# Performance work log

Measured on AMD Instinct MI355X. Metric: run time of the kernel, lower is better.

## Reference

```python
import jax, jax.numpy as jnp
import numpy as np

N = 100000
E = 1000000
P = 1000000
HID = 128
ROLE_VOCAB = 8
ROLE_DIM = 16
IDX_VOCAB = 1024
IDX_DIM = 8
FEAT = 14
IN_DIM = FEAT + IDX_DIM + ROLE_DIM  # 38


def setup_inputs() -> dict:
    key = jax.random.key(0)
    ks = jax.random.split(key, 20)
    s = 0.02
    return {
        "block_features": jax.random.normal(ks[0], (N, FEAT), jnp.float32),
        "role_ids": jax.random.randint(ks[1], (N,), 0, ROLE_VOCAB),
        "b2b_src": jax.random.randint(ks[2], (E,), 0, N),
        "b2b_dst": jax.random.randint(ks[3], (E,), 0, N),
        "b2b_w": jax.random.uniform(ks[4], (E,), jnp.float32),
        "p2b_block": jax.random.randint(ks[5], (P,), 0, N),
        "p2b_w": jax.random.uniform(ks[6], (P,), jnp.float32),
        "role_emb": jax.random.normal(ks[7], (ROLE_VOCAB, ROLE_DIM), jnp.float32),
        "idx_emb": jax.random.normal(ks[8], (IDX_VOCAB, IDX_DIM), jnp.float32),
        "W1": jax.random.normal(ks[9], (IN_DIM, HID), jnp.float32) * s,
        "b1": jnp.zeros((HID,), jnp.float32),
        "W2": jax.random.normal(ks[10], (HID, HID), jnp.float32) * s,
        "b2": jnp.zeros((HID,), jnp.float32),
        "M1": jax.random.normal(ks[11], (HID, HID), jnp.float32) * s,
        "mb1": jnp.zeros((HID,), jnp.float32),
        "M2": jax.random.normal(ks[12], (HID, HID), jnp.float32) * s,
        "mb2": jnp.zeros((HID,), jnp.float32),
        "ln_g": jnp.ones((HID,), jnp.float32),
        "ln_b": jnp.zeros((HID,), jnp.float32),
    }


def _layernorm(x, g, b, eps=1e-5):
    mu = jnp.mean(x, axis=-1, keepdims=True)
    var = jnp.mean(jnp.square(x - mu), axis=-1, keepdims=True)
    return (x - mu) * jax.lax.rsqrt(var + eps) * g + b


def reference(block_features, role_ids, b2b_src, b2b_dst, b2b_w, p2b_block, p2b_w,
              role_emb, idx_emb, W1, b1, W2, b2, M1, mb1, M2, mb2, ln_g, ln_b):
    n = block_features.shape[0]
    # embeddings + input MLP
    re = role_emb[role_ids]                                  # [N, 16]
    ie = idx_emb[jnp.arange(n) % IDX_VOCAB]                  # [N, 8]
    x = jnp.concatenate([block_features, re, ie], axis=-1)   # [N, 38]
    h = jax.nn.relu(x @ W1 + b1)
    emb = jax.nn.relu(h @ W2 + b2)                           # [N, HID]
    # b2b: symmetric weighted scatter-add of neighbor embeddings
    agg = jnp.zeros_like(emb)
    agg = agg.at[b2b_src].add(emb[b2b_dst] * b2b_w[:, None])
    agg = agg.at[b2b_dst].add(emb[b2b_src] * b2b_w[:, None])
    # p2b: agg[j] += emb[j] * w  ==  emb * (sum of pin weights per block)
    pw = jnp.zeros((n,), emb.dtype).at[p2b_block].add(p2b_w)
    agg = agg + emb * pw[:, None]
    # message MLP + residual + LayerNorm
    m = jax.nn.relu(agg @ M1 + mb1) @ M2 + mb2
    block_embeddings = _layernorm(emb + m, ln_g, ln_b)
    graph_embedding = jnp.mean(block_embeddings, axis=0)
    return block_embeddings, graph_embedding
```

## Files before the change

### kernel.cpp

```cpp
#include <hip/hip_runtime.h>

#define FEAT 14
#define ROLE_DIM 16
#define IDX_DIM 8
#define IN_DIM 38
#define HID 128
#define IDX_VOCAB 1024
#define BINN 128
#define NBINS_MAX 800
#define NSEG 1024
#define BINP_CAPT 8
#define BINP_SCAP 16
#define SORT_CAP 4096

typedef __attribute__((ext_vector_type(8))) short short8;
typedef __attribute__((ext_vector_type(4))) float f32x4;
typedef __attribute__((ext_vector_type(2))) float f32x2;

__device__ __forceinline__ ushort f2bf(float f) {
    uint u = __float_as_uint(f);
    return (ushort)((u + 0x7FFFu + ((u >> 16) & 1u)) >> 16);
}
__device__ __forceinline__ float bf2f(ushort h) {
    return __uint_as_float((uint)h << 16);
}
__device__ __forceinline__ uchar f2fp8(float f) {
    return (uchar)(__builtin_amdgcn_cvt_pk_fp8_f32(f, f, 0, false) & 0xff);
}

__global__ void k_prep(const float* __restrict__ W1, const float* __restrict__ W2,
                       const float* __restrict__ M1, const float* __restrict__ M2,
                       ushort* __restrict__ W1t, ushort* __restrict__ W2t,
                       ushort* __restrict__ M1t, ushort* __restrict__ M2t)
{
    int t = blockIdx.x * 256 + threadIdx.x;
    if (t < 8192) {
        int c = t >> 6, k = t & 63;
        W1t[t] = (k < IN_DIM) ? f2bf(W1[k * HID + c]) : (ushort)0;
    } else if (t < 24576) {
        int u = t - 8192; int c = u >> 7, k = u & 127;
        W2t[u] = f2bf(W2[k * HID + c]);
    } else if (t < 40960) {
        int u = t - 24576; int c = u >> 7, k = u & 127;
        M1t[u] = f2bf(M1[k * HID + c]);
    } else if (t < 57344) {
        int u = t - 40960; int c = u >> 7, k = u & 127;
        M2t[u] = f2bf(M2[k * HID + c]);
    }
}

#define LDSA 32768

__device__ __forceinline__ void embed_body(
    char* lds, int id,
    const float* __restrict__ feat, const int* __restrict__ role_ids,
    const float* __restrict__ role_emb, const float* __restrict__ idx_emb,
    const ushort* __restrict__ W1t, const float* __restrict__ b1,
    const ushort* __restrict__ W2t, const float* __restrict__ b2,
    ushort* __restrict__ embh, uchar* __restrict__ embf8, int N)
{
    const int tid = threadIdx.x;
    const int w = tid >> 6, l = tid & 63;
    const int li = l & 15, hi = l >> 4;
    const int base = id * 64;

    for (int c = 0; c < 4; ++c) {
        int idx = c * 256 + tid;
        int col = idx >> 3, ch = idx & 7;
        uint4 v = *(const uint4*)(W1t + col * 64 + ch * 8);
        *(uint4*)(lds + col * 256 + ((ch * 16) ^ ((col & 7) << 4))) = v;
    }
    {
        int row = tid >> 2, kq = (tid & 3) * 16;
        int gr = base + row; if (gr >= N) gr = N - 1;
        int rid = role_ids[gr];
        float xv[16];
        #pragma unroll
        for (int j = 0; j < 16; ++j) {
            int k = kq + j;
            float v = 0.0f;
            if (k < FEAT)                 v = feat[gr * FEAT + k];
            else if (k < FEAT + ROLE_DIM) v = role_emb[rid * ROLE_DIM + (k - FEAT)];
            else if (k < IN_DIM)          v = idx_emb[(gr & (IDX_VOCAB - 1)) * IDX_DIM + (k - FEAT - ROLE_DIM)];
            xv[j] = v;
        }
        uint p[8];
        #pragma unroll
        for (int j = 0; j < 8; ++j)
            p[j] = (uint)f2bf(xv[2 * j]) | ((uint)f2bf(xv[2 * j + 1]) << 16);
        char* db = lds + LDSA + row * 256;
        int sw = (row & 7) << 4;
        *(uint4*)(db + ((kq * 2) ^ sw))      = make_uint4(p[0], p[1], p[2], p[3]);
        *(uint4*)(db + ((kq * 2 + 16) ^ sw)) = make_uint4(p[4], p[5], p[6], p[7]);
    }
    __syncthreads();

    f32x4 C[8];
    #pragma unroll
    for (int ct = 0; ct < 8; ++ct) C[ct] = (f32x4){0.f, 0.f, 0.f, 0.f};
    {
        const int arow = w * 16 + li;
        const int asw = (arow & 7) << 4;
        #pragma unroll
        for (int ks = 0; ks < 2; ++ks) {
            short8 a = *(short8*)(lds + LDSA + arow * 256 + ((ks * 64 + hi * 16) ^ asw));
            #pragma unroll
            for (int ct = 0; ct < 8; ++ct) {
                int bcol = ct * 16 + li;
                short8 b = *(short8*)(lds + bcol * 256 + ((ks * 64 + hi * 16) ^ ((bcol & 7) << 4)));
                C[ct] = __builtin_amdgcn_mfma_f32_16x16x32_bf16(a, b, C[ct], 0, 0, 0);
            }
        }
    }
    __syncthreads();

    #pragma unroll
    for (int ct = 0; ct < 8; ++ct) {
        int col = ct * 16 + li;
        float bv = b1[col];
        #pragma unroll
        for (int r = 0; r < 4; ++r) {
            int hrow = w * 16 + hi * 4 + r;
            float h = fmaxf(C[ct][r] + bv, 0.0f);
            *(ushort*)(lds + LDSA + hrow * 256 + ((col * 2) ^ ((hrow & 7) << 4))) = f2bf(h);
        }
    }
    for (int c = 0; c < 8; ++c) {
        int idx = c * 256 + tid;
        int col = idx >> 4, ch = idx & 15;
        uint4 v = *(const uint4*)(W2t + col * 128 + ch * 8);
        *(uint4*)(lds + col * 256 + ((ch * 16) ^ ((col & 7) << 4))) = v;
    }
    __syncthreads();

    f32x4 C2[8];
    #pragma unroll
    for (int ct = 0; ct < 8; ++ct) C2[ct] = (f32x4){0.f, 0.f, 0.f, 0.f};
    {
        const int arow = w * 16 + li;
        const int asw = (arow & 7) << 4;
        #pragma unroll
        for (int ks = 0; ks < 4; ++ks) {
            short8 a = *(short8*)(lds + LDSA + arow * 256 + ((ks * 64 + hi * 16) ^ asw));
            #pragma unroll
            for (int ct = 0; ct < 8; ++ct) {
                int bcol = ct * 16 + li;
                short8 b = *(short8*)(lds + bcol * 256 + ((ks * 64 + hi * 16) ^ ((bcol & 7) << 4)));
                C2[ct] = __builtin_amdgcn_mfma_f32_16x16x32_bf16(a, b, C2[ct], 0, 0, 0);
            }
        }
    }

    #pragma unroll
    for (int ct = 0; ct < 8; ++ct) {
        int col = ct * 16 + li;
        float bv = b2[col];
        #pragma unroll
        for (int r = 0; r < 4; ++r) {
            int gr = base + w * 16 + hi * 4 + r;
            if (gr < N) {
                float o = fmaxf(C2[ct][r] + bv, 0.0f);
                embh[(size_t)gr * 128 + col] = f2bf(o);
                embf8[(size_t)gr * 128 + col] = f2fp8(o);
            }
        }
    }
}

__device__ __forceinline__ void binp_body(
    char* lds, int id,
    const int* __restrict__ src, const int* __restrict__ dst,
    const float* __restrict__ wgt, uint* __restrict__ staged,
    int* __restrict__ cnt,
    const int* __restrict__ pb, const float* __restrict__ pv,
    float* __restrict__ pw,
    int E, int P, int nbins, int chunkE, int chunkP)
{
    uint* buf   = (uint*)lds;
    int* curT   = (int*)(lds + 25600);
    const int tid = threadIdx.x;
    for (int i = tid; i < nbins; i += 256) curT[i] = 0;
    __syncthreads();

    const int lo = id * chunkE;
    const int hiE = (lo + chunkE) < E ? (lo + chunkE) : E;
    for (int i = lo + tid; i < hiE; i += 256) {
        int s = src[i], d = dst[i];
        uint q = (uint)(wgt[i] * 255.0f + 0.5f);
        int bs = s >> 7;
        uint es = ((uint)(s & 127) << 25) | ((uint)d << 8) | q;
        int ps = atomicAdd(&curT[bs], 1);
        if (ps < BINP_CAPT) buf[bs * BINP_CAPT + ps] = es;
        else if (ps < BINP_SCAP)
            staged[((size_t)bs * NSEG + id) * BINP_SCAP + ps] = es;
        int bd = d >> 7;
        uint ed = ((uint)(d & 127) << 25) | ((uint)s << 8) | q;
        int pd = atomicAdd(&curT[bd], 1);
        if (pd < BINP_CAPT) buf[bd * BINP_CAPT + pd] = ed;
        else if (pd < BINP_SCAP)
            staged[((size_t)bd * NSEG + id) * BINP_SCAP + pd] = ed;
    }
    __syncthreads();
    for (int b = tid; b < nbins; b += 256) {
        int tot = curT[b];
        int k = tot < BINP_CAPT ? tot : BINP_CAPT;
        uint* dp = staged + ((size_t)b * NSEG + id) * BINP_SCAP;
        for (int i = 0; i < k; ++i) dp[i] = buf[b * BINP_CAPT + i];
        cnt[id * nbins + b] = tot < BINP_SCAP ? tot : BINP_SCAP;
    }

    int loP = id * chunkP;
    int hiP = loP + chunkP; if (hiP > P) hiP = P;
    for (int i = loP + tid; i < hiP; i += 256)
        atomicAdd(&pw[pb[i]], pv[i]);
}

__global__ __launch_bounds__(256) void k_embed_binp(
    const float* __restrict__ feat, const int* __restrict__ role_ids,
    const float* __restrict__ role_emb, const float* __restrict__ idx_emb,
    const ushort* __restrict__ W1t, const float* __restrict__ b1,
    const ushort* __restrict__ W2t, const float* __restrict__ b2,
    ushort* __restrict__ embh, uchar* __restrict__ embf8,
    const int* __restrict__ src, const int* __restrict__ dst,
    const float* __restrict__ wgt, uint* __restrict__ staged,
    int* __restrict__ cnt,
    const int* __restrict__ pb, const float* __restrict__ pv,
    float* __restrict__ pw,
    int N, int E, int P, int nbins, int chunkE, int chunkP)
{
    __shared__ char lds[49152];
    const int bid = blockIdx.x;
    int role, id;
    if (bid < 2 * NSEG) { role = bid & 1; id = bid >> 1; }
    else                { role = 0; id = NSEG + (bid - 2 * NSEG); }

    if (role == 0)
        embed_body(lds, id, feat, role_ids, role_emb, idx_emb,
                   W1t, b1, W2t, b2, embh, embf8, N);
    else
        binp_body(lds, id, src, dst, wgt, staged, cnt, pb, pv, pw,
                  E, P, nbins, chunkE, chunkP);
}

__global__ __launch_bounds__(256) void k_agg(
    const uint* __restrict__ staged, const int* __restrict__ cnt,
    const ushort* __restrict__ embh, const uchar* __restrict__ embf8,
    const float* __restrict__ pw,
    ushort* __restrict__ aggh, int N, int nbins)
{
    __shared__ int hist[BINN];
    __shared__ int startL[BINN];
    __shared__ int curL[BINN];
    __shared__ int sc[BINN];
    __shared__ uint sorted[SORT_CAP];

    const int tid = threadIdx.x;
    const int b = blockIdx.x;
    const int baseNode = b << 7;

    if (tid < BINN) hist[tid] = 0;
    __syncthreads();

    int cSeg[4];
    #pragma unroll
    for (int ss = 0; ss < 4; ++ss) {
        int seg = ss * 256 + tid;
        cSeg[ss] = cnt[seg * nbins + b];
        const uint* sp = staged + ((size_t)b * NSEG + seg) * BINP_SCAP;
        for (int k = 0; k < cSeg[ss]; ++k)
            atomicAdd(&hist[sp[k] >> 25], 1);
    }
    __syncthreads();

    int v = (tid < BINN) ? hist[tid] : 0;
    if (tid < BINN) sc[tid] = v;
    __syncthreads();
    for (int off = 1; off < BINN; off <<= 1) {
        int u = (tid < BINN && tid >= off) ? sc[tid - off] : 0;
        __syncthreads();
        if (tid < BINN) sc[tid] += u;
        __syncthreads();
    }
    if (tid < BINN) {
        startL[tid] = sc[tid] - v;
        curL[tid]   = sc[tid] - v;
    }
    __syncthreads();

    #pragma unroll
    for (int ss = 0; ss < 4; ++ss) {
        int seg = ss * 256 + tid;
        const uint* sp = staged + ((size_t)b * NSEG + seg) * BINP_SCAP;
        for (int k = 0; k < cSeg[ss]; ++k) {
            uint e = sp[k];
            int pos = atomicAdd(&curL[e >> 25], 1);
            if (pos < SORT_CAP) sorted[pos] = e;
        }
    }
    __syncthreads();

    const int g  = tid >> 3;
    const int cg = tid & 7;
    const int c0 = cg * 16;
    for (int h = 0; h < 4; ++h) {
        int nl = h * 32 + g;
        int node = baseNode + nl;
        if (node < N) {
            float acc[16];
            float pwn = pw[node];
            const uint4* r = (const uint4*)(embh + ((size_t)node << 7) + c0);
            uint4 u0 = r[0], u1 = r[1];
            uint uu[8] = {u0.x, u0.y, u0.z, u0.w, u1.x, u1.y, u1.z, u1.w};
            #pragma unroll
            for (int j = 0; j < 8; ++j) {
                acc[2*j]   = __uint_as_float(uu[j] << 16) * pwn;
                acc[2*j+1] = __uint_as_float(uu[j] & 0xffff0000u) * pwn;
            }
            const int st = startL[nl], deg = hist[nl];
            #pragma unroll 4
            for (int i = 0; i < deg; ++i) {
                uint en = sorted[st + i];
                int nb   = (int)((en >> 8) & 0x1FFFFu);
                float wt = (float)(en & 255u) * (1.0f / 255.0f);
                uint4 q = *(const uint4*)(embf8 + ((size_t)nb << 7) + c0);
                uint qq[4] = {q.x, q.y, q.z, q.w};
                #pragma unroll
                for (int j = 0; j < 4; ++j) {
                    f32x2 lo = __builtin_amdgcn_cvt_pk_f32_fp8(qq[j], false);
                    f32x2 hi2 = __builtin_amdgcn_cvt_pk_f32_fp8(qq[j], true);
                    acc[4*j+0] = fmaf(lo.x,  wt, acc[4*j+0]);
                    acc[4*j+1] = fmaf(lo.y,  wt, acc[4*j+1]);
                    acc[4*j+2] = fmaf(hi2.x, wt, acc[4*j+2]);
                    acc[4*j+3] = fmaf(hi2.y, wt, acc[4*j+3]);
                }
            }
            uint p[8];
            #pragma unroll
            for (int j = 0; j < 8; ++j)
                p[j] = (uint)f2bf(acc[2*j]) | ((uint)f2bf(acc[2*j+1]) << 16);
            uint4* ap = (uint4*)(aggh + ((size_t)node << 7) + c0);
            ap[0] = make_uint4(p[0], p[1], p[2], p[3]);
            ap[1] = make_uint4(p[4], p[5], p[6], p[7]);
        }
    }
}

#define LDSS 49152

__global__ __launch_bounds__(256) void k_msg_ln(
    const ushort* __restrict__ aggh, const ushort* __restrict__ embh,
    const ushort* __restrict__ M1t, const ushort* __restrict__ M2t,
    const float* __restrict__ mb1, const float* __restrict__ mb2,
    const float* __restrict__ ln_g, const float* __restrict__ ln_b,
    float* __restrict__ out, float* __restrict__ gsum, int N)
{
    __shared__ char lds[51200];
    const int tid = threadIdx.x;
    const int w = tid >> 6, l = tid & 63;
    const int li = l & 15, hi = l >> 4;
    const int base = blockIdx.x * 64;

    for (int c = 0; c < 8; ++c) {
        int idx = c * 256 + tid;
        int col = idx >> 4, ch = idx & 15;
        uint4 v = *(const uint4*)(M1t + col * 128 + ch * 8);
        *(uint4*)(lds + col * 256 + ((ch * 16) ^ ((col & 7) << 4))) = v;
    }
    for (int c = 0; c < 4; ++c) {
        int idx = c * 256 + tid;
        int row = idx >> 4, ch = idx & 15;
        int gr = base + row; if (gr >= N) gr = N - 1;
        uint4 v = *(const uint4*)(aggh + (size_t)gr * 128 + ch * 8);
        *(uint4*)(lds + LDSA + row * 256 + ((ch * 16) ^ ((row & 7) << 4))) = v;
    }
    __syncthreads();

    f32x4 C[8];
    #pragma unroll
    for (int ct = 0; ct < 8; ++ct) C[ct] = (f32x4){0.f, 0.f, 0.f, 0.f};
    {
        const int arow = w * 16 + li;
        const int asw = (arow & 7) << 4;
        #pragma unroll
        for (int ks = 0; ks < 4; ++ks) {
            short8 a = *(short8*)(lds + LDSA + arow * 256 + ((ks * 64 + hi * 16) ^ asw));
            #pragma unroll
            for (int ct = 0; ct < 8; ++ct) {
                int bcol = ct * 16 + li;
                short8 b = *(short8*)(lds + bcol * 256 + ((ks * 64 + hi * 16) ^ ((bcol & 7) << 4)));
                C[ct] = __builtin_amdgcn_mfma_f32_16x16x32_bf16(a, b, C[ct], 0, 0, 0);
            }
        }
    }
    __syncthreads();

    #pragma unroll
    for (int ct = 0; ct < 8; ++ct) {
        int col = ct * 16 + li;
        float bv = mb1[col];
        #pragma unroll
        for (int r = 0; r < 4; ++r) {
            int hrow = w * 16 + hi * 4 + r;
            float h = fmaxf(C[ct][r] + bv, 0.0f);
            *(ushort*)(lds + LDSA + hrow * 256 + ((col * 2) ^ ((hrow & 7) << 4))) = f2bf(h);
        }
    }
    for (int c = 0; c < 8; ++c) {
        int idx = c * 256 + tid;
        int col = idx >> 4, ch = idx & 15;
        uint4 v = *(const uint4*)(M2t + col * 128 + ch * 8);
        *(uint4*)(lds + col * 256 + ((ch * 16) ^ ((col & 7) << 4))) = v;
    }
    __syncthreads();

    f32x4 C2[8];
    #pragma unroll
    for (int ct = 0; ct < 8; ++ct) C2[ct] = (f32x4){0.f, 0.f, 0.f, 0.f};
    {
        const int arow = w * 16 + li;
        const int asw = (arow & 7) << 4;
        #pragma unroll
        for (int ks = 0; ks < 4; ++ks) {
            short8 a = *(short8*)(lds + LDSA + arow * 256 + ((ks * 64 + hi * 16) ^ asw));
            #pragma unroll
            for (int ct = 0; ct < 8; ++ct) {
                int bcol = ct * 16 + li;
                short8 b = *(short8*)(lds + bcol * 256 + ((ks * 64 + hi * 16) ^ ((bcol & 7) << 4)));
                C2[ct] = __builtin_amdgcn_mfma_f32_16x16x32_bf16(a, b, C2[ct], 0, 0, 0);
            }
        }
    }

    float y[8][4];
    #pragma unroll
    for (int ct = 0; ct < 8; ++ct) {
        int col = ct * 16 + li;
        float bv = mb2[col];
        #pragma unroll
        for (int r = 0; r < 4; ++r) {
            int gr = base + w * 16 + hi * 4 + r;
            int grc = gr < N ? gr : N - 1;
            y[ct][r] = C2[ct][r] + bv + bf2f(embh[(size_t)grc * 128 + col]);
        }
    }
    float rs[4] = {0, 0, 0, 0}, rq[4] = {0, 0, 0, 0};
    #pragma unroll
    for (int ct = 0; ct < 8; ++ct)
        #pragma unroll
        for (int r = 0; r < 4; ++r) { rs[r] += y[ct][r]; rq[r] += y[ct][r] * y[ct][r]; }
    #pragma unroll
    for (int m = 1; m < 16; m <<= 1) {
        #pragma unroll
        for (int r = 0; r < 4; ++r) {
            rs[r] += __shfl_xor(rs[r], m);
            rq[r] += __shfl_xor(rq[r], m);
        }
    }
    float mu[4], rstd[4];
    #pragma unroll
    for (int r = 0; r < 4; ++r) {
        mu[r] = rs[r] * (1.0f / HID);
        float var = rq[r] * (1.0f / HID) - mu[r] * mu[r];
        rstd[r] = rsqrtf(var + 1e-5f);
    }
    float cs[8];
    #pragma unroll
    for (int ct = 0; ct < 8; ++ct) {
        cs[ct] = 0.0f;
        int col = ct * 16 + li;
        float g = ln_g[col], bb = ln_b[col];
        #pragma unroll
        for (int r = 0; r < 4; ++r) {
            int gr = base + w * 16 + hi * 4 + r;
            float o = (y[ct][r] - mu[r]) * rstd[r] * g + bb;
            if (gr < N) {
                out[(size_t)gr * 128 + col] = o;
                cs[ct] += o;
            }
        }
    }
    #pragma unroll
    for (int m = 16; m < 64; m <<= 1) {
        #pragma unroll
        for (int ct = 0; ct < 8; ++ct) cs[ct] += __shfl_xor(cs[ct], m);
    }
    float* wsum = (float*)(lds + LDSS);
    if (hi == 0) {
        #pragma unroll
        for (int ct = 0; ct < 8; ++ct) wsum[w * 128 + ct * 16 + li] = cs[ct];
    }
    __syncthreads();
    if (tid < 128) {
        float s = wsum[tid] + wsum[128 + tid] + wsum[256 + tid] + wsum[384 + tid];
        atomicAdd(&gsum[tid], s);
    }
}

__global__ void k_graph(const float* __restrict__ gsum, float* __restrict__ out,
                        int N)
{
    int j = threadIdx.x;
    out[(size_t)N * HID + j] = gsum[j] * (1.0f / (float)N);
}

extern "C" void kernel_launch(void* const* d_in, const int* in_sizes, int n_in,
                              void* d_out, int out_size, void* d_ws, size_t ws_size,
                              hipStream_t stream)
{
    const float* feat      = (const float*)d_in[0];
    const int*   role_ids  = (const int*)  d_in[1];
    const int*   b2b_src   = (const int*)  d_in[2];
    const int*   b2b_dst   = (const int*)  d_in[3];
    const float* b2b_w     = (const float*)d_in[4];
    const int*   p2b_block = (const int*)  d_in[5];
    const float* p2b_w     = (const float*)d_in[6];
    const float* role_emb  = (const float*)d_in[7];
    const float* idx_emb   = (const float*)d_in[8];
    const float* W1        = (const float*)d_in[9];
    const float* b1        = (const float*)d_in[10];
    const float* W2        = (const float*)d_in[11];
    const float* b2        = (const float*)d_in[12];
    const float* M1        = (const float*)d_in[13];
    const float* mb1       = (const float*)d_in[14];
    const float* M2        = (const float*)d_in[15];
    const float* mb2       = (const float*)d_in[16];
    const float* ln_g      = (const float*)d_in[17];
    const float* ln_b      = (const float*)d_in[18];

    const int N = in_sizes[1];
    const int E = in_sizes[2];
    const int P = in_sizes[5];

    float* out = (float*)d_out;

    const int nbins = (N + BINN - 1) >> 7;
    const int chunkE = (E + NSEG - 1) / NSEG;
    const int chunkP = (P + NSEG - 1) / NSEG;

    char* ws = (char*)d_ws;
    size_t embhBytes = (size_t)N * HID * sizeof(ushort);
    size_t embf8Bytes= (size_t)N * HID;
    size_t stagBytes = (size_t)nbins * NSEG * BINP_SCAP * sizeof(uint);
    size_t cntBytes  = (((size_t)NSEG * nbins * sizeof(int)) + 15) & ~15ull;
    size_t vecBytes  = (size_t)N * sizeof(float);

    ushort* embh    = (ushort*)ws;  ws += embhBytes;
    ushort* aggh    = (ushort*)ws;  ws += embhBytes;
    uchar*  embf8   = (uchar*)ws;   ws += embf8Bytes;
    uint*   staged  = (uint*)ws;    ws += stagBytes;
    int*    cnt     = (int*)ws;     ws += cntBytes;
    float*  pw      = (float*)ws;   ws += vecBytes;
    float*  gsum    = (float*)ws;   ws += 512;
    ushort* W1t     = (ushort*)ws;  ws += 8192  * sizeof(ushort);
    ushort* W2t     = (ushort*)ws;  ws += 16384 * sizeof(ushort);
    ushort* M1t     = (ushort*)ws;  ws += 16384 * sizeof(ushort);
    ushort* M2t     = (ushort*)ws;  ws += 16384 * sizeof(ushort);

    hipMemsetAsync(pw, 0, vecBytes + 512, stream);

    const int nEmbed = (N + 63) / 64;

    k_prep<<<224, 256, 0, stream>>>(W1, W2, M1, M2, W1t, W2t, M1t, M2t);

    k_embed_binp<<<nEmbed + NSEG, 256, 0, stream>>>(
        feat, role_ids, role_emb, idx_emb, W1t, b1, W2t, b2, embh, embf8,
        b2b_src, b2b_dst, b2b_w, staged, cnt, p2b_block, p2b_w, pw,
        N, E, P, nbins, chunkE, chunkP);

    k_agg<<<nbins, 256, 0, stream>>>(staged, cnt, embh, embf8, pw, aggh,
                                     N, nbins);

    k_msg_ln<<<(N + 63) / 64, 256, 0, stream>>>(
        aggh, embh, M1t, M2t, mb1, mb2, ln_g, ln_b, out, gsum, N);

    k_graph<<<1, HID, 0, stream>>>(gsum, out, N);
}
```

Baseline: 222.3 us.

## Reduce binning segments to 256 and tile edge binning through LDS

Edge binning now uses 256 segments instead of 1024. Each segment processes its edge chunk in tiles of 2048, flushing per-bin LDS buffers to global staging after each tile and tracking a running per-bin offset. The aggregation kernel then reads one segment per thread instead of four. This aims to cut the per-segment overheads (count writes, sparse staging reads, segment-loop work) at the cost of fewer, longer-running binning blocks and extra syncs per tile. Larger per-segment capacity (64) is needed and may increase staging memory.

After: 229.1 us. +3.1%, slower.

```diff
diff --git a/kernel.cpp b/kernel.cpp
--- a/kernel.cpp
+++ b/kernel.cpp
@@ -8,9 +8,10 @@
 #define IDX_VOCAB 1024
 #define BINN 128
 #define NBINS_MAX 800
-#define NSEG 1024
-#define BINP_CAPT 8
-#define BINP_SCAP 16
+#define NSEG 256
+#define TILE_E 2048
+#define BINP_CAPT 12
+#define BINP_SCAP 64
 #define SORT_CAP 4096
 
 typedef __attribute__((ext_vector_type(8))) short short8;
@@ -176,38 +177,48 @@
     float* __restrict__ pw,
     int E, int P, int nbins, int chunkE, int chunkP)
 {
-    uint* buf   = (uint*)lds;
-    int* curT   = (int*)(lds + 25600);
+    uint* buf    = (uint*)lds;
+    int*  curT   = (int*)(lds + 38400);
+    int*  segCur = (int*)(lds + 41600);
     const int tid = threadIdx.x;
-    for (int i = tid; i < nbins; i += 256) curT[i] = 0;
+    for (int i = tid; i < nbins; i += 256) { curT[i] = 0; segCur[i] = 0; }
     __syncthreads();
 
     const int lo = id * chunkE;
     const int hiE = (lo + chunkE) < E ? (lo + chunkE) : E;
-    for (int i = lo + tid; i < hiE; i += 256) {
-        int s = src[i], d = dst[i];
-        uint q = (uint)(wgt[i] * 255.0f + 0.5f);
-        int bs = s >> 7;
-        uint es = ((uint)(s & 127) << 25) | ((uint)d << 8) | q;
-        int ps = atomicAdd(&curT[bs], 1);
-        if (ps < BINP_CAPT) buf[bs * BINP_CAPT + ps] = es;
-        else if (ps < BINP_SCAP)
-            staged[((size_t)bs * NSEG + id) * BINP_SCAP + ps] = es;
-        int bd = d >> 7;
-        uint ed = ((uint)(d & 127) << 25) | ((uint)s << 8) | q;
-        int pd = atomicAdd(&curT[bd], 1);
-        if (pd < BINP_CAPT) buf[bd * BINP_CAPT + pd] = ed;
-        else if (pd < BINP_SCAP)
-            staged[((size_t)bd * NSEG + id) * BINP_SCAP + pd] = ed;
-    }
-    __syncthreads();
-    for (int b = tid; b < nbins; b += 256) {
-        int tot = curT[b];
-        int k = tot < BINP_CAPT ? tot : BINP_CAPT;
-        uint* dp = staged + ((size_t)b * NSEG + id) * BINP_SCAP;
-        for (int i = 0; i < k; ++i) dp[i] = buf[b * BINP_CAPT + i];
-        cnt[id * nbins + b] = tot < BINP_SCAP ? tot : BINP_SCAP;
-    }
+    for (int t0 = lo; t0 < hiE; t0 += TILE_E) {
+        int t1 = t0 + TILE_E; if (t1 > hiE) t1 = hiE;
+        for (int i = t0 + tid; i < t1; i += 256) {
+            int s = src[i], d = dst[i];
+            uint q = (uint)(wgt[i] * 255.0f + 0.5f);
+            int bs = s >> 7;
+            uint es = ((uint)(s & 127) << 25) | ((uint)d << 8) | q;
+            int ps = atomicAdd(&curT[bs], 1);
+            if (ps < BINP_CAPT) buf[bs * BINP_CAPT + ps] = es;
+            else { int gp = segCur[bs] + ps;
+                   if (gp < BINP_SCAP) staged[((size_t)bs * NSEG + id) * BINP_SCAP + gp] = es; }
+            int bd = d >> 7;
+            uint ed = ((uint)(d & 127) << 25) | ((uint)s << 8) | q;
+            int pd = atomicAdd(&curT[bd], 1);
+            if (pd < BINP_CAPT) buf[bd * BINP_CAPT + pd] = ed;
+            else { int gp = segCur[bd] + pd;
+                   if (gp < BINP_SCAP) staged[((size_t)bd * NSEG + id) * BINP_SCAP + gp] = ed; }
+        }
+        __syncthreads();
+        for (int b = tid; b < nbins; b += 256) {
+            int tot = curT[b];
+            int base = segCur[b];
+            int k = tot < BINP_CAPT ? tot : BINP_CAPT;
+            if (base + k > BINP_SCAP) { k = BINP_SCAP - base; if (k < 0) k = 0; }
+            uint* dp = staged + ((size_t)b * NSEG + id) * BINP_SCAP + base;
+            for (int i = 0; i < k; ++i) dp[i] = buf[b * BINP_CAPT + i];
+            segCur[b] = base + tot;
+            curT[b] = 0;
+        }
+        __syncthreads();
+    }
+    for (int i = tid; i < nbins; i += 256)
+        cnt[id * nbins + i] = segCur[i] < BINP_SCAP ? segCur[i] : BINP_SCAP;
 
     int loP = id * chunkP;
     int hiP = loP + chunkP; if (hiP > P) hiP = P;
@@ -261,15 +272,10 @@
     if (tid < BINN) hist[tid] = 0;
     __syncthreads();
 
-    int cSeg[4];
-    #pragma unroll
-    for (int ss = 0; ss < 4; ++ss) {
-        int seg = ss * 256 + tid;
-        cSeg[ss] = cnt[seg * nbins + b];
-        const uint* sp = staged + ((size_t)b * NSEG + seg) * BINP_SCAP;
-        for (int k = 0; k < cSeg[ss]; ++k)
-            atomicAdd(&hist[sp[k] >> 25], 1);
-    }
+    const int c = cnt[tid * nbins + b];
+    const uint* sp = staged + ((size_t)b * NSEG + tid) * BINP_SCAP;
+    for (int k = 0; k < c; ++k)
+        atomicAdd(&hist[sp[k] >> 25], 1);
     __syncthreads();
 
     int v = (tid < BINN) ? hist[tid] : 0;
@@ -287,15 +293,10 @@
     }
     __syncthreads();
 
-    #pragma unroll
-    for (int ss = 0; ss < 4; ++ss) {
-        int seg = ss * 256 + tid;
-        const uint* sp = staged + ((size_t)b * NSEG + seg) * BINP_SCAP;
-        for (int k = 0; k < cSeg[ss]; ++k) {
-            uint e = sp[k];
-            int pos = atomicAdd(&curL[e >> 25], 1);
-            if (pos < SORT_CAP) sorted[pos] = e;
-        }
+    for (int k = 0; k < c; ++k) {
+        uint e = sp[k];
+        int pos = atomicAdd(&curL[e >> 25], 1);
+        if (pos < SORT_CAP) sorted[pos] = e;
     }
     __syncthreads();
 
```
